# Kernel tuning notes

Measured on AMD Instinct MI355X. Metric: run time of the kernel, lower is better.

## Reference

```python
import jax, jax.numpy as jnp
import numpy as np

BINS = 64
EPS = 1e-8


def _compute_histogram(gray, bins=BINS):
    # gray: [B, H, W] -> normalized histogram [B, bins]
    B = gray.shape[0]
    flat = gray.reshape(B, -1)                      # [B, N]
    mn = flat.min(axis=1, keepdims=True)
    mx = flat.max(axis=1, keepdims=True)
    valid = mx > mn                                  # [B, 1]
    norm = (flat - mn) / jnp.where(valid, mx - mn, 1.0)
    idx = jnp.clip((norm * (bins - 1)).astype(jnp.int32), 0, bins - 1)  # [B, N]
    # per-image bincount via scatter-add
    hist = jax.vmap(lambda i: jnp.zeros(bins, dtype=flat.dtype).at[i].add(1.0))(idx)
    hist = hist / hist.sum(axis=1, keepdims=True)
    return jnp.where(valid, hist, jnp.full_like(hist, 1.0 / bins))


def reference(x, y, lambda_cc=10.0):
    # channel balance
    x_mean = jnp.mean(x, axis=(2, 3), keepdims=True)   # [B,3,1,1]
    y_mean = jnp.mean(y, axis=(2, 3), keepdims=True)
    x_bal = x_mean / (jnp.sum(x_mean, axis=1, keepdims=True) + EPS)
    y_bal = y_mean / (jnp.sum(y_mean, axis=1, keepdims=True) + EPS)
    color_balance_loss = jnp.mean(jnp.abs(x_bal - y_bal))

    # luminance
    x_gray = 0.299 * x[:, 0] + 0.587 * x[:, 1] + 0.114 * x[:, 2]  # [B,H,W]
    y_gray = 0.299 * y[:, 0] + 0.587 * y[:, 1] + 0.114 * y[:, 2]

    x_hist = _compute_histogram(x_gray)
    y_hist = _compute_histogram(y_gray)

    # F.kl_div(log(x_hist+eps), y_hist, reduction='batchmean')
    log_in = jnp.log(x_hist + EPS)
    ylogy = jnp.where(y_hist > 0, y_hist * jnp.log(jnp.where(y_hist > 0, y_hist, 1.0)), 0.0)
    kl = jnp.sum(ylogy - y_hist * log_in) / x.shape[0]

    return lambda_cc * (color_balance_loss + kl)


def setup_inputs() -> dict:
    key = jax.random.key(0)
    k1, k2 = jax.random.split(key)
    x = jax.random.uniform(k1, (16, 3, 512, 512), dtype=jnp.float32)
    y = jax.random.uniform(k2, (16, 3, 512, 512), dtype=jnp.float32)
    return {"x": x, "y": y}
```

## Files before the change

### kernel.cpp

```cpp
#include <hip/hip_runtime.h>

#define HW_N (512 * 512)
#define BINS 64
#define BPI 64
#define TPB 256

struct ImgStats {
    double sumx[3];
    double sumy[3];
    unsigned int minx, maxx, miny, maxy;
    unsigned int histx[BINS];
    unsigned int histy[BINS];
};

__device__ __forceinline__ unsigned int f2ord(float f) {
    unsigned int u = __float_as_uint(f);
    return (u & 0x80000000u) ? ~u : (u | 0x80000000u);
}
__device__ __forceinline__ float ord2f(unsigned int u) {
    u = (u & 0x80000000u) ? (u ^ 0x80000000u) : ~u;
    return __uint_as_float(u);
}

__device__ __forceinline__ float grayf(float r, float g, float b) {
    return 0.299f * r + 0.587f * g + 0.114f * b;
}

__device__ __forceinline__ double waveSumD(double v) {
#pragma unroll
    for (int o = 32; o > 0; o >>= 1) v += __shfl_down(v, o);
    return v;
}
__device__ __forceinline__ float waveMinF(float v) {
#pragma unroll
    for (int o = 32; o > 0; o >>= 1) v = fminf(v, __shfl_down(v, o));
    return v;
}
__device__ __forceinline__ float waveMaxF(float v) {
#pragma unroll
    for (int o = 32; o > 0; o >>= 1) v = fmaxf(v, __shfl_down(v, o));
    return v;
}

__global__ void k_init(ImgStats* st, int B) {
    const int nwords = B * (int)(sizeof(ImgStats) / 4);
    unsigned int* w = (unsigned int*)st;
    for (int i = threadIdx.x; i < nwords; i += blockDim.x) w[i] = 0u;
    __syncthreads();
    for (int i = threadIdx.x; i < B * 2; i += blockDim.x) {
        int b = i >> 1;
        if (i & 1) st[b].miny = 0xFFFFFFFFu;
        else       st[b].minx = 0xFFFFFFFFu;
    }
}

__global__ __launch_bounds__(TPB) void k_reduce(const float* __restrict__ x,
                                                const float* __restrict__ y,
                                                ImgStats* __restrict__ st) {
    const int b   = blockIdx.x / BPI;
    const int sub = blockIdx.x % BPI;
    const int qPerBlock = (HW_N / 4) / BPI;
    const int q0 = sub * qPerBlock;
    const size_t base = (size_t)b * 3 * HW_N;

    const float4* xr = (const float4*)(x + base);
    const float4* xg = (const float4*)(x + base + HW_N);
    const float4* xb = (const float4*)(x + base + 2 * HW_N);
    const float4* yr = (const float4*)(y + base);
    const float4* yg = (const float4*)(y + base + HW_N);
    const float4* yb = (const float4*)(y + base + 2 * HW_N);

    float s0 = 0.f, s1 = 0.f, s2 = 0.f;
    float t0 = 0.f, t1 = 0.f, t2 = 0.f;
    float mnx = 3.4e38f, mxx = -3.4e38f;
    float mny = 3.4e38f, mxy = -3.4e38f;

    for (int i = threadIdx.x; i < qPerBlock; i += TPB) {
        const int q = q0 + i;
        float4 r = xr[q], g = xg[q], bl = xb[q];
        s0 += (r.x + r.y) + (r.z + r.w);
        s1 += (g.x + g.y) + (g.z + g.w);
        s2 += (bl.x + bl.y) + (bl.z + bl.w);
        {
            float g0 = grayf(r.x, g.x, bl.x), g1 = grayf(r.y, g.y, bl.y);
            float g2 = grayf(r.z, g.z, bl.z), g3 = grayf(r.w, g.w, bl.w);
            mnx = fminf(mnx, fminf(fminf(g0, g1), fminf(g2, g3)));
            mxx = fmaxf(mxx, fmaxf(fmaxf(g0, g1), fmaxf(g2, g3)));
        }
        r = yr[q]; g = yg[q]; bl = yb[q];
        t0 += (r.x + r.y) + (r.z + r.w);
        t1 += (g.x + g.y) + (g.z + g.w);
        t2 += (bl.x + bl.y) + (bl.z + bl.w);
        {
            float g0 = grayf(r.x, g.x, bl.x), g1 = grayf(r.y, g.y, bl.y);
            float g2 = grayf(r.z, g.z, bl.z), g3 = grayf(r.w, g.w, bl.w);
            mny = fminf(mny, fminf(fminf(g0, g1), fminf(g2, g3)));
            mxy = fmaxf(mxy, fmaxf(fmaxf(g0, g1), fmaxf(g2, g3)));
        }
    }

    const int wave = threadIdx.x >> 6;
    const int lane = threadIdx.x & 63;
    __shared__ double shs[6][TPB / 64];
    __shared__ float  shmn[2][TPB / 64];
    __shared__ float  shmx[2][TPB / 64];

    double d;
    d = waveSumD((double)s0); if (!lane) shs[0][wave] = d;
    d = waveSumD((double)s1); if (!lane) shs[1][wave] = d;
    d = waveSumD((double)s2); if (!lane) shs[2][wave] = d;
    d = waveSumD((double)t0); if (!lane) shs[3][wave] = d;
    d = waveSumD((double)t1); if (!lane) shs[4][wave] = d;
    d = waveSumD((double)t2); if (!lane) shs[5][wave] = d;
    float f;
    f = waveMinF(mnx); if (!lane) shmn[0][wave] = f;
    f = waveMinF(mny); if (!lane) shmn[1][wave] = f;
    f = waveMaxF(mxx); if (!lane) shmx[0][wave] = f;
    f = waveMaxF(mxy); if (!lane) shmx[1][wave] = f;
    __syncthreads();

    if (threadIdx.x == 0) {
        atomicAdd(&st[b].sumx[0], shs[0][0] + shs[0][1] + shs[0][2] + shs[0][3]);
        atomicAdd(&st[b].sumx[1], shs[1][0] + shs[1][1] + shs[1][2] + shs[1][3]);
        atomicAdd(&st[b].sumx[2], shs[2][0] + shs[2][1] + shs[2][2] + shs[2][3]);
        atomicAdd(&st[b].sumy[0], shs[3][0] + shs[3][1] + shs[3][2] + shs[3][3]);
        atomicAdd(&st[b].sumy[1], shs[4][0] + shs[4][1] + shs[4][2] + shs[4][3]);
        atomicAdd(&st[b].sumy[2], shs[5][0] + shs[5][1] + shs[5][2] + shs[5][3]);
        float a;
        a = fminf(fminf(shmn[0][0], shmn[0][1]), fminf(shmn[0][2], shmn[0][3]));
        atomicMin(&st[b].minx, f2ord(a));
        a = fminf(fminf(shmn[1][0], shmn[1][1]), fminf(shmn[1][2], shmn[1][3]));
        atomicMin(&st[b].miny, f2ord(a));
        a = fmaxf(fmaxf(shmx[0][0], shmx[0][1]), fmaxf(shmx[0][2], shmx[0][3]));
        atomicMax(&st[b].maxx, f2ord(a));
        a = fmaxf(fmaxf(shmx[1][0], shmx[1][1]), fmaxf(shmx[1][2], shmx[1][3]));
        atomicMax(&st[b].maxy, f2ord(a));
    }
}

__global__ __launch_bounds__(TPB) void k_hist(const float* __restrict__ x,
                                              const float* __restrict__ y,
                                              ImgStats* __restrict__ st) {
    __shared__ unsigned int lh[8][BINS];
    for (int i = threadIdx.x; i < 8 * BINS; i += TPB) ((unsigned int*)lh)[i] = 0u;

    const int b   = blockIdx.x / BPI;
    const int sub = blockIdx.x % BPI;

    const float mnx = ord2f(st[b].minx), mxx = ord2f(st[b].maxx);
    const float mny = ord2f(st[b].miny), mxy = ord2f(st[b].maxy);
    const float rgx = (mxx > mnx) ? (mxx - mnx) : 1.0f;
    const float rgy = (mxy > mny) ? (mxy - mny) : 1.0f;
    __syncthreads();

    const int qPerBlock = (HW_N / 4) / BPI;
    const int q0 = sub * qPerBlock;
    const size_t base = (size_t)b * 3 * HW_N;

    const float4* xr = (const float4*)(x + base);
    const float4* xg = (const float4*)(x + base + HW_N);
    const float4* xb = (const float4*)(x + base + 2 * HW_N);
    const float4* yr = (const float4*)(y + base);
    const float4* yg = (const float4*)(y + base + HW_N);
    const float4* yb = (const float4*)(y + base + 2 * HW_N);

    const int wave = threadIdx.x >> 6;
    unsigned int* hx = lh[wave];
    unsigned int* hy = lh[4 + wave];

    for (int i = threadIdx.x; i < qPerBlock; i += TPB) {
        const int q = q0 + i;
        float4 r = xr[q], g = xg[q], bl = xb[q];
        {
            float gv[4] = { grayf(r.x, g.x, bl.x), grayf(r.y, g.y, bl.y),
                            grayf(r.z, g.z, bl.z), grayf(r.w, g.w, bl.w) };
#pragma unroll
            for (int j = 0; j < 4; j++) {
                float t = ((gv[j] - mnx) / rgx) * 63.0f;
                int id = (int)t;
                id = id < 0 ? 0 : (id > 63 ? 63 : id);
                atomicAdd(&hx[id], 1u);
            }
        }
        r = yr[q]; g = yg[q]; bl = yb[q];
        {
            float gv[4] = { grayf(r.x, g.x, bl.x), grayf(r.y, g.y, bl.y),
                            grayf(r.z, g.z, bl.z), grayf(r.w, g.w, bl.w) };
#pragma unroll
            for (int j = 0; j < 4; j++) {
                float t = ((gv[j] - mny) / rgy) * 63.0f;
                int id = (int)t;
                id = id < 0 ? 0 : (id > 63 ? 63 : id);
                atomicAdd(&hy[id], 1u);
            }
        }
    }
    __syncthreads();

    for (int i = threadIdx.x; i < 2 * BINS; i += TPB) {
        const int src = i >> 6, bin = i & 63;
        unsigned int v = lh[src * 4 + 0][bin] + lh[src * 4 + 1][bin] +
                         lh[src * 4 + 2][bin] + lh[src * 4 + 3][bin];
        if (v) atomicAdd(src ? &st[b].histy[bin] : &st[b].histx[bin], v);
    }
}

__global__ __launch_bounds__(1024) void k_final(const ImgStats* __restrict__ st,
                                                float* __restrict__ out, int B) {
    const int tid = threadIdx.x;
    double klt = 0.0, cbt = 0.0;

    for (int t = tid; t < B * BINS; t += 1024) {
        const int b = t >> 6, bin = t & 63;
        const ImgStats& s = st[b];
        const float mnx = ord2f(s.minx), mxx = ord2f(s.maxx);
        const float mny = ord2f(s.miny), mxy = ord2f(s.maxy);
        const float invN = 1.0f / (float)HW_N;
        const float xh = (mxx > mnx) ? (float)s.histx[bin] * invN : (1.0f / BINS);
        const float yh = (mxy > mny) ? (float)s.histy[bin] * invN : (1.0f / BINS);
        const float log_in = logf(xh + 1e-8f);
        const float ylogy = (yh > 0.0f) ? yh * logf(yh) : 0.0f;
        klt += (double)ylogy - (double)yh * (double)log_in;
    }

    for (int t = tid; t < B * 3; t += 1024) {
        const int b = t / 3, c = t % 3;
        const ImgStats& s = st[b];
        const double N = (double)HW_N;
        const double xb = (s.sumx[c] / N) /
                          ((s.sumx[0] + s.sumx[1] + s.sumx[2]) / N + 1e-8);
        const double yb = (s.sumy[c] / N) /
                          ((s.sumy[0] + s.sumy[1] + s.sumy[2]) / N + 1e-8);
        cbt += fabs(xb - yb);
    }

    __shared__ double skl[16], scb[16];
    const double kw = waveSumD(klt);
    const double cw = waveSumD(cbt);
    const int wave = tid >> 6, lane = tid & 63;
    if (!lane) { skl[wave] = kw; scb[wave] = cw; }
    __syncthreads();
    if (tid == 0) {
        double K = 0.0, C = 0.0;
        for (int i = 0; i < 16; i++) { K += skl[i]; C += scb[i]; }
        const double kl = K / (double)B;
        const double cb = C / (double)(B * 3);
        out[0] = (float)(10.0 * (cb + kl));
    }
}

extern "C" void kernel_launch(void* const* d_in, const int* in_sizes, int n_in,
                              void* d_out, int out_size, void* d_ws, size_t ws_size,
                              hipStream_t stream) {
    const float* x = (const float*)d_in[0];
    const float* y = (const float*)d_in[1];
    float* out = (float*)d_out;
    const int B = in_sizes[0] / (3 * HW_N);

    ImgStats* st = (ImgStats*)d_ws;

    k_init<<<1, 256, 0, stream>>>(st, B);
    k_reduce<<<B * BPI, TPB, 0, stream>>>(x, y, st);
    k_hist<<<B * BPI, TPB, 0, stream>>>(x, y, st);
    k_final<<<1, 1024, 0, stream>>>(st, out, B);
}
```

Baseline: 140.4 us.

## Materialize grayscale in reduce pass and histogram from gray buffers

The reduce kernel now writes the per-pixel luminance of x and y to workspace buffers while computing sums and min/max. A new histogram kernel then reads only these gray values instead of re-reading all three RGB channels, which cuts the second pass's reads by roughly two thirds. It also spreads shared-memory atomics over 16 sub-histograms, one per half-wave per image. The cost is an extra write of the gray buffers in the first pass. The fallback path for a small workspace still writes gray values into a possibly undersized buffer, which is a correctness risk.

```diff
diff --git a/kernel.cpp b/kernel.cpp
--- a/kernel.cpp
+++ b/kernel.cpp
@@ -54,14 +54,17 @@
     }
 }
 
-__global__ __launch_bounds__(TPB) void k_reduce(const float* __restrict__ x,
-                                                const float* __restrict__ y,
-                                                ImgStats* __restrict__ st) {
+__global__ __launch_bounds__(TPB) void k_reduce_gray(const float* __restrict__ x,
+                                                     const float* __restrict__ y,
+                                                     ImgStats* __restrict__ st,
+                                                     float4* __restrict__ gx,
+                                                     float4* __restrict__ gy) {
     const int b   = blockIdx.x / BPI;
     const int sub = blockIdx.x % BPI;
     const int qPerBlock = (HW_N / 4) / BPI;
     const int q0 = sub * qPerBlock;
     const size_t base = (size_t)b * 3 * HW_N;
+    const size_t gbase = (size_t)b * (HW_N / 4);
 
     const float4* xr = (const float4*)(x + base);
     const float4* xg = (const float4*)(x + base + HW_N);
@@ -82,20 +85,22 @@
         s1 += (g.x + g.y) + (g.z + g.w);
         s2 += (bl.x + bl.y) + (bl.z + bl.w);
         {
-            float g0 = grayf(r.x, g.x, bl.x), g1 = grayf(r.y, g.y, bl.y);
-            float g2 = grayf(r.z, g.z, bl.z), g3 = grayf(r.w, g.w, bl.w);
-            mnx = fminf(mnx, fminf(fminf(g0, g1), fminf(g2, g3)));
-            mxx = fmaxf(mxx, fmaxf(fmaxf(g0, g1), fmaxf(g2, g3)));
+            float4 gv = make_float4(grayf(r.x, g.x, bl.x), grayf(r.y, g.y, bl.y),
+                                    grayf(r.z, g.z, bl.z), grayf(r.w, g.w, bl.w));
+            gx[gbase + q] = gv;
+            mnx = fminf(mnx, fminf(fminf(gv.x, gv.y), fminf(gv.z, gv.w)));
+            mxx = fmaxf(mxx, fmaxf(fmaxf(gv.x, gv.y), fmaxf(gv.z, gv.w)));
         }
         r = yr[q]; g = yg[q]; bl = yb[q];
         t0 += (r.x + r.y) + (r.z + r.w);
         t1 += (g.x + g.y) + (g.z + g.w);
         t2 += (bl.x + bl.y) + (bl.z + bl.w);
         {
-            float g0 = grayf(r.x, g.x, bl.x), g1 = grayf(r.y, g.y, bl.y);
-            float g2 = grayf(r.z, g.z, bl.z), g3 = grayf(r.w, g.w, bl.w);
-            mny = fminf(mny, fminf(fminf(g0, g1), fminf(g2, g3)));
-            mxy = fmaxf(mxy, fmaxf(fmaxf(g0, g1), fmaxf(g2, g3)));
+            float4 gv = make_float4(grayf(r.x, g.x, bl.x), grayf(r.y, g.y, bl.y),
+                                    grayf(r.z, g.z, bl.z), grayf(r.w, g.w, bl.w));
+            gy[gbase + q] = gv;
+            mny = fminf(mny, fminf(fminf(gv.x, gv.y), fminf(gv.z, gv.w)));
+            mxy = fmaxf(mxy, fmaxf(fmaxf(gv.x, gv.y), fmaxf(gv.z, gv.w)));
         }
     }
 
@@ -138,6 +143,61 @@
     }
 }
 
+__global__ __launch_bounds__(TPB) void k_hist_gray(const float4* __restrict__ gx,
+                                                   const float4* __restrict__ gy,
+                                                   ImgStats* __restrict__ st) {
+    __shared__ unsigned int lh[16][BINS];
+    for (int i = threadIdx.x; i < 16 * BINS; i += TPB) ((unsigned int*)lh)[i] = 0u;
+
+    const int b   = blockIdx.x / BPI;
+    const int sub = blockIdx.x % BPI;
+
+    const float mnx = ord2f(st[b].minx), mxx = ord2f(st[b].maxx);
+    const float mny = ord2f(st[b].miny), mxy = ord2f(st[b].maxy);
+    const float rgx = (mxx > mnx) ? (mxx - mnx) : 1.0f;
+    const float rgy = (mxy > mny) ? (mxy - mny) : 1.0f;
+    __syncthreads();
+
+    const int qPerBlock = (HW_N / 4) / BPI;
+    const int q0 = sub * qPerBlock;
+    const size_t gbase = (size_t)b * (HW_N / 4);
+
+    const int wave = threadIdx.x >> 6;
+    const int half = (threadIdx.x >> 5) & 1;
+    unsigned int* hx = lh[wave * 2 + half];
+    unsigned int* hy = lh[8 + wave * 2 + half];
+
+    for (int i = threadIdx.x; i < qPerBlock; i += TPB) {
+        const float4 gvx = gx[gbase + q0 + i];
+        const float4 gvy = gy[gbase + q0 + i];
+        const float vx[4] = { gvx.x, gvx.y, gvx.z, gvx.w };
+        const float vy[4] = { gvy.x, gvy.y, gvy.z, gvy.w };
+#pragma unroll
+        for (int j = 0; j < 4; j++) {
+            float t = ((vx[j] - mnx) / rgx) * 63.0f;
+            int id = (int)t;
+            id = id < 0 ? 0 : (id > 63 ? 63 : id);
+            atomicAdd(&hx[id], 1u);
+        }
+#pragma unroll
+        for (int j = 0; j < 4; j++) {
+            float t = ((vy[j] - mny) / rgy) * 63.0f;
+            int id = (int)t;
+            id = id < 0 ? 0 : (id > 63 ? 63 : id);
+            atomicAdd(&hy[id], 1u);
+        }
+    }
+    __syncthreads();
+
+    for (int i = threadIdx.x; i < 2 * BINS; i += TPB) {
+        const int src = i >> 6, bin = i & 63;
+        unsigned int v = 0;
+#pragma unroll
+        for (int k = 0; k < 8; k++) v += lh[src * 8 + k][bin];
+        if (v) atomicAdd(src ? &st[b].histy[bin] : &st[b].histx[bin], v);
+    }
+}
+
 __global__ __launch_bounds__(TPB) void k_hist(const float* __restrict__ x,
                                               const float* __restrict__ y,
                                               ImgStats* __restrict__ st) {
@@ -259,8 +319,22 @@
 
     ImgStats* st = (ImgStats*)d_ws;
 
+    const size_t grayBytes = (size_t)B * HW_N * sizeof(float);
+    const size_t grayOff   = 16384;
+    const size_t needed    = grayOff + 2 * grayBytes;
+
     k_init<<<1, 256, 0, stream>>>(st, B);
-    k_reduce<<<B * BPI, TPB, 0, stream>>>(x, y, st);
-    k_hist<<<B * BPI, TPB, 0, stream>>>(x, y, st);
+
+    if (ws_size >= needed) {
+        float4* gx = (float4*)((char*)d_ws + grayOff);
+        float4* gy = (float4*)((char*)d_ws + grayOff + grayBytes);
+        k_reduce_gray<<<B * BPI, TPB, 0, stream>>>(x, y, st, gx, gy);
+        k_hist_gray<<<B * BPI, TPB, 0, stream>>>(gx, gy, st);
+    } else {
+        k_reduce_gray<<<B * BPI, TPB, 0, stream>>>(x, y, st,
+            (float4*)((char*)d_ws + grayOff), (float4*)((char*)d_ws + grayOff));
+        k_hist<<<B * BPI, TPB, 0, stream>>>(x, y, st);
+    }
+
     k_final<<<1, 1024, 0, stream>>>(st, out, B);
 }
```

New measurement: 141.4 us. No clear change (+0.7%).
